# Kernel optimization log

Measured on AMD Instinct MI355X. Metric: run time of the kernel, lower is better.

The kernel has to match this reference:

```python
import math
import jax, jax.numpy as jnp
import numpy as np

CHUNK = 32
EPS = 1e-5


def l2norm(x):
    return x * jax.lax.rsqrt(jnp.sum(x * x, -1, keepdims=True))


def causal_dwconv(x, w):
    # x: (B, C, L); w: (C, K) depthwise causal conv (left pad K-1)
    C, K = w.shape
    return jax.lax.conv_general_dilated(x, w[:, None, :], (1,), [(K - 1, 0)], feature_group_count=C)


def per_head_stats(x):
    # x: (B,L,H,D) -> (B,L,H,4): mean, var(pop), abs-mean, l2-norm
    mean = jnp.mean(x, -1, keepdims=True)
    var = jnp.mean(x * x, -1, keepdims=True) - mean * mean
    abs_mean = jnp.mean(jnp.abs(x), -1, keepdims=True)
    l2 = jnp.sqrt(jnp.sum(x * x, -1, keepdims=True))
    return jnp.concatenate([mean, var, abs_mean, l2], -1)


def delta_rule_chunkwise(q, k, v, beta, chunk=CHUNK):
    # q,k: (B,H,L,dk); v: (B,H,L,dv); beta: (B,H,L)
    b, h, L, dk = q.shape
    dv = v.shape[-1]
    pad = (-L) % chunk
    if pad:
        pc = ((0, 0), (0, 0), (0, pad), (0, 0))
        q, k, v = (jnp.pad(t, pc) for t in (q, k, v))
        beta = jnp.pad(beta, ((0, 0), (0, 0), (0, pad)))
    Lp = L + pad
    n = Lp // chunk
    q = l2norm(q)
    k = l2norm(k)
    v = v * beta[..., None]
    kb = k * beta[..., None]
    resh = lambda t: t.reshape(b, h, n, chunk, t.shape[-1])
    q, k, v, kb = map(resh, (q, k, v, kb))
    tri = jnp.triu(jnp.ones((chunk, chunk), bool))          # incl. diag
    strict = jnp.triu(jnp.ones((chunk, chunk), bool), 1)    # above diag
    A = jnp.where(tri, 0.0, -jnp.einsum('bhncd,bhned->bhnce', kb, k))
    # forward-substitution inverse of (I - strict_lower) as in the torch loop
    for i in range(1, chunk):
        upd = jnp.einsum('...k,...kj->...j', A[..., i, :], A[..., :, :i])
        A = A.at[..., i, :i].add(upd)
    inv = A + jnp.eye(chunk, dtype=A.dtype)
    u = inv @ v   # (b,h,n,c,dv)
    w = inv @ kb  # (b,h,n,c,dk)

    def step(S, xs):
        qi, ki, ui, wi = xs  # (b,h,c,d)
        attn = jnp.where(strict, 0.0, qi @ jnp.swapaxes(ki, -1, -2))
        u_adj = ui - wi @ S
        out_i = qi @ S + attn @ u_adj
        S = S + jnp.swapaxes(ki, -1, -2) @ u_adj
        return S, out_i

    xs = tuple(jnp.moveaxis(t, 2, 0) for t in (q, k, u, w))
    S0 = jnp.zeros((b, h, dk, dv), q.dtype)
    S, outs = jax.lax.scan(step, S0, xs)
    out = jnp.moveaxis(outs, 0, 2).reshape(b, h, Lp, dv)[:, :, :L]
    return out, S


def reference(hidden_states, q_proj_w, k_proj_w, v_proj_w, b_proj_w,
              q_conv_w, k_conv_w, v_conv_w, fir_short_w, fir_long_w,
              fuse_w1, fuse_b1, fuse_w2, fuse_b2, logit_temp,
              res_scale_short, res_scale_long, o_norm_w, o_proj_w):
    B, L, D = hidden_states.shape
    H = fir_short_w.shape[0]

    def shortconv(x, w):  # x: (B,L,C)
        y = causal_dwconv(jnp.swapaxes(x, 1, 2), w)
        return jax.nn.silu(jnp.swapaxes(y, 1, 2))

    q = shortconv(hidden_states @ q_proj_w.T, q_conv_w)
    k = shortconv(hidden_states @ k_proj_w.T, k_conv_w)
    v = shortconv(hidden_states @ v_proj_w.T, v_conv_w)
    q = q.reshape(B, L, H, -1)
    k = k.reshape(B, L, H, -1)
    v_direct = v.reshape(B, L, H, -1)
    beta = jax.nn.sigmoid(hidden_states @ b_proj_w.T)  # (B,L,H)

    delta_out, _S = delta_rule_chunkwise(
        jnp.transpose(q, (0, 2, 1, 3)), jnp.transpose(k, (0, 2, 1, 3)),
        jnp.transpose(v_direct, (0, 2, 1, 3)), jnp.transpose(beta, (0, 2, 1)))
    delta_out = jnp.transpose(delta_out, (0, 2, 1, 3))

    def fir(x, filt):  # x: (B,L,H,Dh); filt: (H,Dh,K)
        hh, dd, kk = filt.shape
        xf = jnp.swapaxes(x.reshape(B, L, hh * dd), 1, 2)
        y = causal_dwconv(xf, filt.reshape(hh * dd, kk))
        return jnp.swapaxes(y, 1, 2).reshape(B, L, hh, dd)

    local_short = fir(v_direct, fir_short_w)
    local_long = fir(v_direct, fir_long_w)

    stats = jnp.concatenate([per_head_stats(t) for t in
                             (local_short, local_long, delta_out, v_direct)], -1)  # (B,L,H,16)
    hs_exp = jnp.broadcast_to(hidden_states[:, :, None, :], (B, L, H, D))
    gate_in = jnp.concatenate([hs_exp, stats], -1)
    hdn = jax.nn.gelu(gate_in @ fuse_w1.T + fuse_b1, approximate=False)
    logits = hdn @ fuse_w2.T + fuse_b2  # (B,L,H,4)
    temp = jax.nn.softplus(logit_temp) + 1e-4
    fw = jax.nn.softmax(logits / temp, -1)

    o = (fw[..., 0:1] * local_short + fw[..., 1:2] * local_long
         + fw[..., 2:3] * delta_out + fw[..., 3:4] * v_direct)
    o = o + res_scale_short * local_short + res_scale_long * local_long
    o = o * jax.lax.rsqrt(jnp.mean(o * o, -1, keepdims=True) + EPS) * o_norm_w
    return o.reshape(B, L, -1) @ o_proj_w.T


def setup_inputs() -> dict:
    key = jax.random.key(0)
    ks = jax.random.split(key, 16)
    B, L, D, H = 2, 4096, 1024, 4
    dk, dv = D, D
    dh = dv // H
    gate_in_dim = D + 16
    gate_hidden = D * 2 // 2
    s = 0.02
    f32 = jnp.float32
    return {
        'hidden_states': jax.random.normal(ks[0], (B, L, D), f32),
        'q_proj_w': jax.random.normal(ks[1], (dk, D), f32) * s,
        'k_proj_w': jax.random.normal(ks[2], (dk, D), f32) * s,
        'v_proj_w': jax.random.normal(ks[3], (dv, D), f32) * s,
        'b_proj_w': jax.random.normal(ks[4], (H, D), f32) * s,
        'q_conv_w': jax.random.normal(ks[5], (dk, 4), f32) * 0.1,
        'k_conv_w': jax.random.normal(ks[6], (dk, 4), f32) * 0.1,
        'v_conv_w': jax.random.normal(ks[7], (dv, 4), f32) * 0.1,
        'fir_short_w': jax.random.normal(ks[8], (H, dh, 5), f32) * 0.02,
        'fir_long_w': jax.random.normal(ks[9], (H, dh, 64), f32) * 0.02,
        'fuse_w1': jax.random.normal(ks[10], (gate_hidden, gate_in_dim), f32) * s,
        'fuse_b1': jnp.zeros((gate_hidden,), f32),
        'fuse_w2': jax.random.normal(ks[11], (4, gate_hidden), f32) * s,
        'fuse_b2': jnp.array([-1.0, -1.0, 1.0, 3.0], f32),
        'logit_temp': jnp.full((1,), math.log(math.expm1(0.7)), f32),
        'res_scale_short': jnp.full((1,), 0.1, f32),
        'res_scale_long': jnp.full((1,), 0.1, f32),
        'o_norm_w': jnp.ones((dh,), f32),
        'o_proj_w': jax.random.normal(ks[12], (D, dv), f32) * s,
    }
```

## Files before the change

### kernel.cpp

```cpp
#include <hip/hip_runtime.h>
#include <hip/hip_bf16.h>

#define BB 2
#define LL 4096
#define DD 1024
#define HH 4
#define DH 256
#define CH 32
#define NC (LL/CH)
#define BL (BB*LL)
#define BLD ((size_t)BB*LL*DD)

typedef __attribute__((ext_vector_type(8))) short short8;
typedef __attribute__((ext_vector_type(4))) float floatx4;

__device__ __forceinline__ float bf2f(unsigned short u) {
    union { float f; unsigned int i; } x; x.i = ((unsigned int)u) << 16; return x.f;
}
__device__ __forceinline__ float bflo(unsigned int u) {
    union { float f; unsigned int i; } x; x.i = u << 16; return x.f;
}
__device__ __forceinline__ float bfhi(unsigned int u) {
    union { float f; unsigned int i; } x; x.i = u & 0xFFFF0000u; return x.f;
}
__device__ __forceinline__ unsigned short f2bf(float f) {
    union { float f; unsigned int i; } x; x.f = f;
    unsigned int r = x.i + 0x7FFFu + ((x.i >> 16) & 1u);
    return (unsigned short)(r >> 16);
}
__device__ __forceinline__ unsigned int pkbf(float a, float b) {
    unsigned int ua = __float_as_uint(a) + 0x8000u;
    unsigned int ub = __float_as_uint(b) + 0x8000u;
    return __builtin_amdgcn_perm(ub, ua, 0x07060302);
}
__device__ __forceinline__ void lds_barrier() {
    __builtin_amdgcn_s_waitcnt(0xC07F);
    __builtin_amdgcn_s_barrier();
}

typedef __attribute__((address_space(1))) const unsigned int as1_uint;
typedef __attribute__((address_space(3))) unsigned int as3_uint;
__device__ __forceinline__ void dma16(const void* g, void* l) {
    __builtin_amdgcn_global_load_lds((as1_uint*)g, (as3_uint*)l, 16, 0, 0);
}

__global__ __launch_bounds__(256) void cvt_bf_k(
    const float* __restrict__ x, unsigned short* __restrict__ y)
{
    size_t i = ((size_t)blockIdx.x * 256 + threadIdx.x) * 4;
    float4 v = *(const float4*)(x + i);
    ushort4 o;
    o.x = f2bf(v.x); o.y = f2bf(v.y); o.z = f2bf(v.z); o.w = f2bf(v.w);
    *(ushort4*)(y + i) = o;
}

__global__ __launch_bounds__(256) void w1s_prep_k(
    const float* __restrict__ w1, unsigned short* __restrict__ w1s)
{
    int idx = blockIdx.x * 256 + threadIdx.x;
    int e = idx >> 4, s = idx & 15;
    w1s[idx] = f2bf(w1[(size_t)e * 1040 + 1024 + s]);
}

__global__ __launch_bounds__(256) void gemm_mfma(
    const float* __restrict__ A, int lda,
    const float* __restrict__ W, int ldw,
    const float* __restrict__ bias,
    float* __restrict__ C, int ldc, int K)
{
    __shared__ unsigned short Abuf[128][56];
    __shared__ unsigned short Bbuf[128][56];
    const int t = threadIdx.x;
    const int wave = t >> 6, lane = t & 63;
    const int wm = wave >> 1, wn = wave & 1;
    const int row0 = blockIdx.y * 128, col0 = blockIdx.x * 128;

    floatx4 acc[4][4];
#pragma unroll
    for (int i = 0; i < 4; ++i)
#pragma unroll
        for (int j = 0; j < 4; ++j) acc[i][j] = (floatx4){0.f, 0.f, 0.f, 0.f};

    const int fr = lane & 15, fk = (lane >> 4) * 8;

    for (int kt = 0; kt < K; kt += 32) {
        __syncthreads();
#pragma unroll
        for (int it = 0; it < 2; ++it) {
            int idx = t + it * 256;
            int r = idx >> 2, s = (idx & 3) * 8;
            const float* ap = A + (size_t)(row0 + r) * lda + kt + s;
            float4 a0 = *(const float4*)(ap);
            float4 a1 = *(const float4*)(ap + 4);
            ushort4 p0, p1;
            p0.x = f2bf(a0.x); p0.y = f2bf(a0.y); p0.z = f2bf(a0.z); p0.w = f2bf(a0.w);
            p1.x = f2bf(a1.x); p1.y = f2bf(a1.y); p1.z = f2bf(a1.z); p1.w = f2bf(a1.w);
            *(ushort4*)&Abuf[r][s]     = p0;
            *(ushort4*)&Abuf[r][s + 4] = p1;
            const float* wp = W + (size_t)(col0 + r) * ldw + kt + s;
            float4 b0 = *(const float4*)(wp);
            float4 b1 = *(const float4*)(wp + 4);
            ushort4 q0, q1;
            q0.x = f2bf(b0.x); q0.y = f2bf(b0.y); q0.z = f2bf(b0.z); q0.w = f2bf(b0.w);
            q1.x = f2bf(b1.x); q1.y = f2bf(b1.y); q1.z = f2bf(b1.z); q1.w = f2bf(b1.w);
            *(ushort4*)&Bbuf[r][s]     = q0;
            *(ushort4*)&Bbuf[r][s + 4] = q1;
        }
        __syncthreads();

        short8 afrag[4], bfrag[4];
#pragma unroll
        for (int i = 0; i < 4; ++i) {
            afrag[i] = *(const short8*)&Abuf[wm * 64 + i * 16 + fr][fk];
            bfrag[i] = *(const short8*)&Bbuf[wn * 64 + i * 16 + fr][fk];
        }
#pragma unroll
        for (int i = 0; i < 4; ++i)
#pragma unroll
            for (int j = 0; j < 4; ++j)
                acc[i][j] = __builtin_amdgcn_mfma_f32_16x16x32_bf16(
                    afrag[i], bfrag[j], acc[i][j], 0, 0, 0);
    }

    const int fc = lane & 15, frow = (lane >> 4) * 4;
#pragma unroll
    for (int j = 0; j < 4; ++j) {
        int col = col0 + wn * 64 + j * 16 + fc;
        float bv = bias ? bias[col] : 0.0f;
#pragma unroll
        for (int i = 0; i < 4; ++i) {
#pragma unroll
            for (int r = 0; r < 4; ++r) {
                int row = row0 + wm * 64 + i * 16 + frow + r;
                C[(size_t)row * ldc + col] = acc[i][j][r] + bv;
            }
        }
    }
}

__global__ __launch_bounds__(256) void gemm_bb(
    const unsigned short* __restrict__ A, int lda,
    const unsigned short* __restrict__ B, int ldb,
    float* __restrict__ C, int ldc, int K)
{
    __shared__ unsigned short Abuf[128][56];
    __shared__ unsigned short Bbuf[128][56];
    const int t = threadIdx.x;
    const int wave = t >> 6, lane = t & 63;
    const int wm = wave >> 1, wn = wave & 1;
    const int row0 = blockIdx.y * 128, col0 = blockIdx.x * 128;

    floatx4 acc[4][4];
#pragma unroll
    for (int i = 0; i < 4; ++i)
#pragma unroll
        for (int j = 0; j < 4; ++j) acc[i][j] = (floatx4){0.f, 0.f, 0.f, 0.f};

    const int fr = lane & 15, fk = (lane >> 4) * 8;

    for (int kt = 0; kt < K; kt += 32) {
        __syncthreads();
#pragma unroll
        for (int it = 0; it < 2; ++it) {
            int idx = t + it * 256;
            int r = idx >> 2, s = (idx & 3) * 8;
            uint4 av = *(const uint4*)(A + (size_t)(row0 + r) * lda + kt + s);
            *(uint4*)&Abuf[r][s] = av;
            uint4 bv = *(const uint4*)(B + (size_t)(col0 + r) * ldb + kt + s);
            *(uint4*)&Bbuf[r][s] = bv;
        }
        __syncthreads();

        short8 afrag[4], bfrag[4];
#pragma unroll
        for (int i = 0; i < 4; ++i) {
            afrag[i] = *(const short8*)&Abuf[wm * 64 + i * 16 + fr][fk];
            bfrag[i] = *(const short8*)&Bbuf[wn * 64 + i * 16 + fr][fk];
        }
#pragma unroll
        for (int i = 0; i < 4; ++i)
#pragma unroll
            for (int j = 0; j < 4; ++j)
                acc[i][j] = __builtin_amdgcn_mfma_f32_16x16x32_bf16(
                    afrag[i], bfrag[j], acc[i][j], 0, 0, 0);
    }

    const int fc = lane & 15, frow = (lane >> 4) * 4;
#pragma unroll
    for (int j = 0; j < 4; ++j) {
        int col = col0 + wn * 64 + j * 16 + fc;
#pragma unroll
        for (int i = 0; i < 4; ++i) {
#pragma unroll
            for (int r = 0; r < 4; ++r) {
                int row = row0 + wm * 64 + i * 16 + frow + r;
                C[(size_t)row * ldc + col] = acc[i][j][r];
            }
        }
    }
}

__global__ __launch_bounds__(256) void convnorm_qk_k(
    const float* __restrict__ x, const float* __restrict__ w,
    unsigned short* __restrict__ y)
{
    int bl = blockIdx.x >> 2;
    int h  = blockIdx.x & 3;
    int l  = bl & (LL - 1);
    int d  = threadIdx.x;
    int c  = h * DH + d;
    const float* wp = w + (size_t)c * 4;
    const float* xp = x + (size_t)bl * DD + c;
    float acc = wp[3] * xp[0];
    if (l >= 1) acc += wp[2] * xp[-(int)DD];
    if (l >= 2) acc += wp[1] * xp[-2*(int)DD];
    if (l >= 3) acc += wp[0] * xp[-3*(int)DD];
    acc = acc / (1.0f + expf(-acc));
    float s = acc * acc;
#pragma unroll
    for (int off = 32; off > 0; off >>= 1) s += __shfl_down(s, off);
    __shared__ float red[4];
    int wv = threadIdx.x >> 6, ln = threadIdx.x & 63;
    if (ln == 0) red[wv] = s;
    __syncthreads();
    float tot = red[0] + red[1] + red[2] + red[3];
    y[(size_t)bl * DD + c] = f2bf(acc * rsqrtf(tot));
}

__global__ __launch_bounds__(256) void conv_silu_k(
    const float* __restrict__ x, const float* __restrict__ w, float* __restrict__ y)
{
    size_t idx = (size_t)blockIdx.x * 256 + threadIdx.x;
    int c = (int)(idx & (DD - 1));
    int bl = (int)(idx >> 10);
    int l = bl & (LL - 1);
    const float* wp = w + (size_t)c * 4;
    const float* xp = x + (size_t)bl * DD + c;
    float acc = wp[3] * xp[0];
    if (l >= 1) acc += wp[2] * xp[-(int)DD];
    if (l >= 2) acc += wp[1] * xp[-2*(int)DD];
    if (l >= 3) acc += wp[0] * xp[-3*(int)DD];
    y[idx] = acc / (1.0f + expf(-acc));
}

template<int K>
__global__ __launch_bounds__(256) void fir2_k(
    const float* __restrict__ x, const float* __restrict__ filt, float* __restrict__ y)
{
    const int ctile = blockIdx.x & 15;
    const int ltile = (blockIdx.x >> 4) & 63;
    const int b = blockIdx.x >> 10;
    const int RT = 64 + K - 1;
    __shared__ float xs[RT][64];
    __shared__ float fs[64][K + 1];
    const int t = threadIdx.x;
    const int l0 = ltile * 64;

    for (int i = t; i < RT * 16; i += 256) {
        int li = i >> 4, c4 = (i & 15) * 4;
        int l = l0 - (K - 1) + li;
        float4 v = make_float4(0.f, 0.f, 0.f, 0.f);
        if (l >= 0)
            v = *(const float4*)(x + ((size_t)b * LL + l) * DD + ctile * 64 + c4);
        *(float4*)&xs[li][c4] = v;
    }
    for (int i = t; i < 64 * K; i += 256) {
        fs[i / K][i % K] = filt[(size_t)ctile * 64 * K + i];
    }
    __syncthreads();

    const int c = t & 63, lg = t >> 6;
    float acc[16];
#pragma unroll
    for (int o = 0; o < 16; ++o) acc[o] = 0.f;
#pragma unroll
    for (int j = 0; j < 16 + K - 1; ++j) {
        float xv = xs[lg * 16 + j][c];
#pragma unroll
        for (int o = 0; o < 16; ++o) {
            int tap = j - o;
            if (tap >= 0 && tap < K) acc[o] += fs[c][tap] * xv;
        }
    }
    size_t base = ((size_t)b * LL + l0 + lg * 16) * DD + ctile * 64 + c;
#pragma unroll
    for (int o = 0; o < 16; ++o)
        y[base + (size_t)o * DD] = acc[o];
}

__global__ __launch_bounds__(256) void beta_k(
    const float* __restrict__ hs, const float* __restrict__ bw, float* __restrict__ beta)
{
    int bl = blockIdx.x;
    const float* xr = hs + (size_t)bl * DD;
    float a0=0.f,a1=0.f,a2=0.f,a3=0.f;
    for (int k = threadIdx.x; k < DD; k += 256) {
        float xv = xr[k];
        a0 += xv * bw[k];
        a1 += xv * bw[DD + k];
        a2 += xv * bw[2*DD + k];
        a3 += xv * bw[3*DD + k];
    }
#pragma unroll
    for (int off = 32; off > 0; off >>= 1) {
        a0 += __shfl_down(a0, off); a1 += __shfl_down(a1, off);
        a2 += __shfl_down(a2, off); a3 += __shfl_down(a3, off);
    }
    __shared__ float red[4][4];
    int wv = threadIdx.x >> 6, ln = threadIdx.x & 63;
    if (ln == 0) { red[wv][0]=a0; red[wv][1]=a1; red[wv][2]=a2; red[wv][3]=a3; }
    __syncthreads();
    if (threadIdx.x < 4) {
        int h = threadIdx.x;
        float s = red[0][h] + red[1][h] + red[2][h] + red[3][h];
        beta[(size_t)bl * HH + h] = 1.0f / (1.0f + expf(-s));
    }
}

__global__ __launch_bounds__(256) void tr_k(
    const unsigned short* __restrict__ k, unsigned short* __restrict__ kT)
{
    int et = blockIdx.x & 3;
    int lt = (blockIdx.x >> 2) & 63;
    int bh = blockIdx.x >> 8;
    int h = bh & 3, b = bh >> 2;
    __shared__ unsigned short tile[64][72];
    int t = threadIdx.x;
    int tr = t >> 4;
    int tc = (t & 15) * 4;
#pragma unroll
    for (int i = 0; i < 4; ++i) {
        int l = tr + i * 16;
        ushort4 v = *(const ushort4*)(k + ((size_t)b * LL + lt*64 + l) * DD + h * DH + et*64 + tc);
        *(ushort4*)&tile[l][tc] = v;
    }
    __syncthreads();
#pragma unroll
    for (int i = 0; i < 4; ++i) {
        int e = tr + i * 16;
        ushort4 v;
        v.x = tile[tc+0][e]; v.y = tile[tc+1][e];
        v.z = tile[tc+2][e]; v.w = tile[tc+3][e];
        *(ushort4*)(kT + ((size_t)bh * DH + et*64 + e) * LL + (size_t)lt*64 + tc) = v;
    }
}

__global__ __launch_bounds__(256) void chunk_prep2_k(
    const unsigned short* __restrict__ q, const unsigned short* __restrict__ k,
    const unsigned short* __restrict__ kT, const float* __restrict__ v,
    const float* __restrict__ beta,
    unsigned short* __restrict__ uT, unsigned short* __restrict__ w_out,
    unsigned short* __restrict__ attn_out)
{
    const int ci = blockIdx.x & (NC - 1);
    const int bh = blockIdx.x >> 7;
    const int h = bh & (HH - 1), b = bh >> 2;
    __shared__ unsigned short kL[32][264];
    __shared__ unsigned short qL[32][264];
    __shared__ float vL[32][260];
    __shared__ float AmL[32][33];
    __shared__ unsigned short AbH[32][40];
    __shared__ unsigned short AbL2[32][40];
    __shared__ float betL[32];
    const int t = threadIdx.x;
    const int wave = t >> 6, lane = t & 63;
    const int lr = lane & 15, lg = lane >> 4;
    const int l0 = ci * CH;
    const size_t rowbase = (size_t)b * LL + l0;

    for (int i = t; i < 1024; i += 256) {
        int r = i >> 5, s8 = (i & 31) * 8;
        *(uint4*)&kL[r][s8] = *(const uint4*)(k + (rowbase + r) * DD + h * DH + s8);
        *(uint4*)&qL[r][s8] = *(const uint4*)(q + (rowbase + r) * DD + h * DH + s8);
    }
    for (int i = t; i < 2048; i += 256) {
        int e = i >> 6, d4 = (i & 63) * 4;
        *(float4*)&vL[e][d4] = *(const float4*)(v + (rowbase + e) * DD + h * DH + d4);
    }
    if (t < 32) betL[t] = beta[(rowbase + t) * HH + h];
    __syncthreads();

    const int mt = wave >> 1, nt = wave & 1;
    floatx4 accA = (floatx4){0.f,0.f,0.f,0.f}, accT = accA;
#pragma unroll
    for (int ks = 0; ks < 8; ++ks) {
        short8 bk = *(const short8*)&kL[nt * 16 + lr][ks * 32 + lg * 8];
        short8 ak = *(const short8*)&kL[mt * 16 + lr][ks * 32 + lg * 8];
        short8 aq = *(const short8*)&qL[mt * 16 + lr][ks * 32 + lg * 8];
        accA = __builtin_amdgcn_mfma_f32_16x16x32_bf16(ak, bk, accA, 0, 0, 0);
        accT = __builtin_amdgcn_mfma_f32_16x16x32_bf16(aq, bk, accT, 0, 0, 0);
    }
    {
        const size_t abase = (size_t)blockIdx.x * (CH * CH);
        const int ee = nt * 16 + lr;
#pragma unroll
        for (int r = 0; r < 4; ++r) {
            int c = mt * 16 + lg * 4 + r;
            float bc = betL[c];
            AmL[c][ee] = (ee < c) ? (-bc * accA[r]) : 0.0f;
            attn_out[abase + (size_t)c * CH + ee] =
                (ee <= c) ? f2bf(accT[r]) : (unsigned short)0;
        }
    }
    __syncthreads();

    const unsigned short* kTg = kT + (size_t)bh * DH * LL;
    short8 wB[4];
#pragma unroll
    for (int n = 0; n < 4; ++n)
        wB[n] = *(const short8*)(kTg + (size_t)(wave * 64 + n * 16 + lr) * LL + l0 + lg * 8);

    if (wave == 0) {
        const int j = lane & 31;
        float col[32];
#pragma unroll
        for (int c = 0; c < 32; ++c) col[c] = AmL[c][j];
#pragma unroll
        for (int i = 1; i < 32; ++i) {
            float u0 = 0.f, u1 = 0.f;
#pragma unroll
            for (int kk = 0; kk < 32; kk += 2) {
                if (kk < i)     u0 += __shfl(col[i], kk) * col[kk];
                if (kk + 1 < i) u1 += __shfl(col[i], kk + 1) * col[kk + 1];
            }
            if (j < i) col[i] += u0 + u1;
        }
        if (lane < 32) {
            const float bj = betL[j];
#pragma unroll
            for (int c = 0; c < 32; ++c) {
                float val = (col[c] + (c == j ? 1.0f : 0.0f)) * bj;
                unsigned short hi = f2bf(val);
                AbH[c][j] = hi;
                AbL2[c][j] = f2bf(val - bf2f(hi));
            }
        }
    }
    __syncthreads();

    short8 AH[2], ALo[2];
#pragma unroll
    for (int m = 0; m < 2; ++m) {
        AH[m]  = *(const short8*)&AbH[m * 16 + lr][lg * 8];
        ALo[m] = *(const short8*)&AbL2[m * 16 + lr][lg * 8];
    }
    const size_t uTbase = (size_t)bh * DH * LL;
    const size_t wbase  = (size_t)bh * LL * DH;
#pragma unroll
    for (int n = 0; n < 4; ++n) {
        const int d = wave * 64 + n * 16 + lr;
        union { short8 s8; unsigned int u[4]; } vf;
#pragma unroll
        for (int p2 = 0; p2 < 4; ++p2)
            vf.u[p2] = pkbf(vL[lg * 8 + p2 * 2][d], vL[lg * 8 + p2 * 2 + 1][d]);
#pragma unroll
        for (int m = 0; m < 2; ++m) {
            floatx4 au = (floatx4){0.f,0.f,0.f,0.f};
            au = __builtin_amdgcn_mfma_f32_16x16x32_bf16(AH[m],  vf.s8, au, 0, 0, 0);
            au = __builtin_amdgcn_mfma_f32_16x16x32_bf16(ALo[m], vf.s8, au, 0, 0, 0);
            ushort4 ou;
            ou.x = f2bf(au[0]); ou.y = f2bf(au[1]); ou.z = f2bf(au[2]); ou.w = f2bf(au[3]);
            *(ushort4*)(uT + uTbase + (size_t)d * LL + l0 + m * 16 + lg * 4) = ou;

            floatx4 aw = (floatx4){0.f,0.f,0.f,0.f};
            aw = __builtin_amdgcn_mfma_f32_16x16x32_bf16(AH[m],  wB[n], aw, 0, 0, 0);
            aw = __builtin_amdgcn_mfma_f32_16x16x32_bf16(ALo[m], wB[n], aw, 0, 0, 0);
#pragma unroll
            for (int r = 0; r < 4; ++r)
                w_out[wbase + (size_t)(l0 + m * 16 + lg * 4 + r) * DH + d] = f2bf(aw[r]);
        }
    }
}

__global__ __launch_bounds__(256, 1) void scan10_k(
    const unsigned short* __restrict__ q, const unsigned short* __restrict__ kT,
    const unsigned short* __restrict__ uT, const unsigned short* __restrict__ w,
    const unsigned short* __restrict__ attn, float* __restrict__ dout)
{
    const int bh = blockIdx.x & 7;
    const int jb = blockIdx.x >> 3;
    const int h = bh & (HH - 1), b = bh >> 2;
    const int jcol = jb * 16;
    const int wave = threadIdx.x >> 6, lane = threadIdx.x & 63;
    const int lr = lane & 15, lg = lane >> 4;
    const int half = wave & 1;
    const bool isQ = wave >= 2;

    #define OW 0
    #define OQ 16384
    #define OK2 32768
    #define OA 49152
    #define OU 51200
    __shared__ char slotmem[2][52224];
    __shared__ unsigned short SbT[2][16][264];
    __shared__ unsigned short uadjT[2][16][40];

    floatx4 Sacc[4];
#pragma unroll
    for (int mt = 0; mt < 4; ++mt) Sacc[mt] = (floatx4){0.f,0.f,0.f,0.f};

    const char* wbB  = (const char*)(w  + (size_t)bh * LL * DH);
    const char* qbB  = (const char*)(q  + (size_t)b * LL * DD + h * DH);
    const char* kbB  = (const char*)(kT + (size_t)bh * DH * LL);
    const char* uTbB = (const char*)(uT + (size_t)bh * DH * LL);
    const char* atB  = (const char*)(attn + (size_t)bh * NC * (CH * CH));
    float* db = dout + (size_t)bh * LL * DH;

    const int lane16 = lane * 16;
    int pw[4], pq[4], pkt[4];
#pragma unroll
    for (int j = 0; j < 4; ++j) {
        int i = wave + 4 * j;
        int L = i * 1024 + lane16;
        { int row = L >> 9, g = (L >> 4) & 31, gs = g ^ (row & 7);
          pw[j] = row * 512 + gs * 16; }
        { int row = L >> 9, g = (L >> 4) & 31, gs = g ^ (row & 7);
          pq[j] = row * 2048 + gs * 16; }
        { int row = L >> 6, g = (L >> 4) & 3, gs = g ^ (row & 3);
          pkt[j] = row * 8192 + gs * 16; }
    }
    int pat = 0, put = 0;
    if (wave < 2) { int L = wave * 1024 + lane16;
        int row = L >> 6, g = (L >> 4) & 3, gs = g ^ (row & 3);
        pat = row * 64 + gs * 16; }
    else if (wave == 2) { int L = lane16;
        int row = L >> 6, g = (L >> 4) & 3;
        put = (jcol + row) * 8192 + g * 16; }

    const int row_o = half * 16 + lr;
    int opo[8];
#pragma unroll
    for (int kt = 0; kt < 8; ++kt)
        opo[kt] = row_o * 512 + (((kt * 4 + lg) ^ (row_o & 7)) * 16);
    int opk[4];
#pragma unroll
    for (int mt = 0; mt < 4; ++mt) {
        int rk = 64 * wave + 16 * mt + lr;
        opk[mt] = rk * 64 + ((lg ^ (rk & 3)) * 16);
    }
    const int opa = row_o * 64 + ((lg ^ (row_o & 3)) * 16);
    const int opu = lr * 64 + half * 32 + lg * 8;

    {
        char* sb = &slotmem[0][0];
#pragma unroll
        for (int j = 0; j < 4; ++j) {
            int i = wave + 4 * j;
            dma16(wbB + pw[j],  sb + OW  + i * 1024);
            dma16(qbB + pq[j],  sb + OQ  + i * 1024);
            dma16(kbB + pkt[j], sb + OK2 + i * 1024);
        }
        if (wave < 2)       dma16(atB + pat,  sb + OA + wave * 1024);
        else if (wave == 2) dma16(uTbB + put, sb + OU);
    }

#pragma unroll 2
    for (int ci = 0; ci < NC; ++ci) {
        const int p = ci & 1;
        const int l0 = ci * CH;

#pragma unroll
        for (int mt = 0; mt < 4; ++mt) {
            int e0 = 64 * wave + 16 * mt + lg * 4;
            *(unsigned int*)&SbT[p][lr][e0]     = pkbf(Sacc[mt][0], Sacc[mt][1]);
            *(unsigned int*)&SbT[p][lr][e0 + 2] = pkbf(Sacc[mt][2], Sacc[mt][3]);
        }

        asm volatile("s_waitcnt vmcnt(0)" ::: "memory");
        lds_barrier();

        {
            const int cn = (ci + 1 < NC) ? (ci + 1) : ci;
            const size_t lnW = (size_t)(cn * CH) * 512;
            const size_t lnQ = (size_t)(cn * CH) * 2048;
            const size_t lnK = (size_t)(cn * CH) * 2;
            char* sb = &slotmem[p ^ 1][0];
#pragma unroll
            for (int j = 0; j < 4; ++j) {
                int i = wave + 4 * j;
                dma16(wbB + lnW + pw[j],  sb + OW  + i * 1024);
                dma16(qbB + lnQ + pq[j],  sb + OQ  + i * 1024);
                dma16(kbB + lnK + pkt[j], sb + OK2 + i * 1024);
            }
            if (wave < 2)       dma16(atB + (size_t)cn * 2048 + pat, sb + OA + wave * 1024);
            else if (wave == 2) dma16(uTbB + lnK + put, sb + OU);
        }

        const char* sp = &slotmem[p][0];
        const char* ab = sp + (isQ ? OQ : OW);

        floatx4 Pa = (floatx4){0.f,0.f,0.f,0.f}, Pb = Pa;
#pragma unroll
        for (int kt = 0; kt < 4; ++kt) {
            short8 s0 = *(const short8*)&SbT[p][lr][(2*kt)   * 32 + lg * 8];
            short8 s1 = *(const short8*)&SbT[p][lr][(2*kt+1) * 32 + lg * 8];
            short8 a0 = *(const short8*)(ab + opo[2*kt]);
            short8 a1 = *(const short8*)(ab + opo[2*kt+1]);
            Pa = __builtin_amdgcn_mfma_f32_16x16x32_bf16(a0, s0, Pa, 0,0,0);
            Pb = __builtin_amdgcn_mfma_f32_16x16x32_bf16(a1, s1, Pb, 0,0,0);
        }
        floatx4 P = Pa + Pb;

        if (!isQ) {
            ushort4 u4 = *(const ushort4*)(sp + OU + opu);
            float ua0 = bf2f(u4.x) - P[0];
            float ua1 = bf2f(u4.y) - P[1];
            float ua2 = bf2f(u4.z) - P[2];
            float ua3 = bf2f(u4.w) - P[3];
            int cc0 = half * 16 + lg * 4;
            *(unsigned int*)&uadjT[p][lr][cc0]     = pkbf(ua0, ua1);
            *(unsigned int*)&uadjT[p][lr][cc0 + 2] = pkbf(ua2, ua3);
        }
        lds_barrier();

        short8 ub = *(const short8*)&uadjT[p][lr][lg * 8];

        if (isQ) {
            short8 paR = *(const short8*)(sp + OA + opa);
            floatx4 Ot = __builtin_amdgcn_mfma_f32_16x16x32_bf16(paR, ub, P, 0,0,0);
#pragma unroll
            for (int r = 0; r < 4; ++r)
                db[(size_t)(l0 + half * 16 + lg * 4 + r) * DH + jcol + lr] = Ot[r];
        }

#pragma unroll
        for (int mt = 0; mt < 4; ++mt) {
            short8 pkR = *(const short8*)(sp + OK2 + opk[mt]);
            Sacc[mt] = __builtin_amdgcn_mfma_f32_16x16x32_bf16(pkR, ub, Sacc[mt], 0,0,0);
        }
    }
    #undef OW
    #undef OQ
    #undef OK2
    #undef OA
    #undef OU
}

__global__ __launch_bounds__(256) void stats_k(
    const float* __restrict__ ls, const float* __restrict__ llb,
    const float* __restrict__ dox, const float* __restrict__ v,
    float* __restrict__ stats)
{
    int bl = blockIdx.x;
    int b = bl >> 12, l = bl & (LL - 1);
    int wv = threadIdx.x >> 6, ln = threadIdx.x & 63;
    size_t ibase = (size_t)bl * DD + wv * DH;
    size_t dbase = (((size_t)(b * HH + wv)) * LL + l) * DH;
#pragma unroll
    for (int tn = 0; tn < 4; ++tn) {
        const float* p; size_t base;
        if (tn == 0)      { p = ls;  base = ibase; }
        else if (tn == 1) { p = llb; base = ibase; }
        else if (tn == 2) { p = dox; base = dbase; }
        else              { p = v;   base = ibase; }
        float4 x = *(const float4*)(p + base + ln * 4);
        float sm = x.x + x.y + x.z + x.w;
        float sq = x.x*x.x + x.y*x.y + x.z*x.z + x.w*x.w;
        float sa = fabsf(x.x) + fabsf(x.y) + fabsf(x.z) + fabsf(x.w);
#pragma unroll
        for (int off = 32; off > 0; off >>= 1) {
            sm += __shfl_down(sm, off);
            sq += __shfl_down(sq, off);
            sa += __shfl_down(sa, off);
        }
        if (ln == 0) {
            float mean = sm * (1.0f / DH);
            float var = sq * (1.0f / DH) - mean * mean;
            float am = sa * (1.0f / DH);
            float l2 = sqrtf(sq);
            *(float4*)(stats + (size_t)bl * 64 + wv * 16 + tn * 4) =
                make_float4(mean, var, am, l2);
        }
    }
}

__global__ __launch_bounds__(256) void gate_fin2_k(
    const float* __restrict__ hpart, const float* __restrict__ stats,
    const unsigned short* __restrict__ w1s,
    const float* __restrict__ w2, const float* __restrict__ b2,
    const float* __restrict__ ltemp, float* __restrict__ fw)
{
    const int bl = blockIdx.x;
    const int t = threadIdx.x;
    const float temp = log1pf(expf(ltemp[0])) + 1e-4f;
    __shared__ float st[HH][16];
    __shared__ float red[4][16];
    __shared__ float fin[16];
    if (t < 64) st[t >> 4][t & 15] = stats[(size_t)bl * 64 + t];

    const int e0 = t * 4;
    float4 hp4 = *(const float4*)(hpart + (size_t)bl * DD + e0);
    float hp[4] = {hp4.x, hp4.y, hp4.z, hp4.w};
    float w2a[4][4];
#pragma unroll
    for (int j = 0; j < 4; ++j) {
        float4 wv = *(const float4*)(w2 + (size_t)j * 1024 + e0);
        w2a[j][0] = wv.x; w2a[j][1] = wv.y; w2a[j][2] = wv.z; w2a[j][3] = wv.w;
    }
    uint4 wpk[8];
    const uint4* wp = (const uint4*)(w1s + (size_t)e0 * 16);
#pragma unroll
    for (int i = 0; i < 8; ++i) wpk[i] = wp[i];
    __syncthreads();

    float lg[4][4];
#pragma unroll
    for (int h = 0; h < 4; ++h)
#pragma unroll
        for (int j = 0; j < 4; ++j) lg[h][j] = 0.0f;

#pragma unroll
    for (int ii = 0; ii < 4; ++ii) {
        float xh[4] = {hp[ii], hp[ii], hp[ii], hp[ii]};
        unsigned arr[8] = {wpk[ii*2].x, wpk[ii*2].y, wpk[ii*2].z, wpk[ii*2].w,
                           wpk[ii*2+1].x, wpk[ii*2+1].y, wpk[ii*2+1].z, wpk[ii*2+1].w};
#pragma unroll
        for (int p = 0; p < 8; ++p) {
            float wlo = bflo(arr[p]), whi = bfhi(arr[p]);
            int s = p * 2;
#pragma unroll
            for (int h = 0; h < 4; ++h)
                xh[h] += st[h][s] * wlo + st[h][s + 1] * whi;
        }
#pragma unroll
        for (int h = 0; h < 4; ++h) {
            float x = xh[h];
            float gct = 0.5f * x * (1.0f + erff(x * 0.70710678118654752f));
            lg[h][0] += gct * w2a[0][ii];
            lg[h][1] += gct * w2a[1][ii];
            lg[h][2] += gct * w2a[2][ii];
            lg[h][3] += gct * w2a[3][ii];
        }
    }

#pragma unroll
    for (int h = 0; h < 4; ++h)
#pragma unroll
        for (int j = 0; j < 4; ++j)
#pragma unroll
            for (int off = 32; off > 0; off >>= 1)
                lg[h][j] += __shfl_down(lg[h][j], off);

    const int wv = t >> 6, ln = t & 63;
    if (ln == 0) {
#pragma unroll
        for (int h = 0; h < 4; ++h)
#pragma unroll
            for (int j = 0; j < 4; ++j) red[wv][h * 4 + j] = lg[h][j];
    }
    __syncthreads();
    if (t < 16) {
        float s = red[0][t] + red[1][t] + red[2][t] + red[3][t] + b2[t & 3];
        fin[t] = s / temp;
    }
    __syncthreads();
    if (t < 4) {
        float l0 = fin[t*4], l1 = fin[t*4+1], l2 = fin[t*4+2], l3 = fin[t*4+3];
        float m = fmaxf(fmaxf(l0, l1), fmaxf(l2, l3));
        float e0x = expf(l0-m), e1 = expf(l1-m), e2 = expf(l2-m), e3 = expf(l3-m);
        float inv = 1.0f / (e0x + e1 + e2 + e3);
        *(float4*)(fw + (size_t)bl * 16 + t * 4) = make_float4(e0x*inv, e1*inv, e2*inv, e3*inv);
    }
}

__global__ __launch_bounds__(256) void combine_k(
    const float* __restrict__ ls, const float* __restrict__ llb,
    const float* __restrict__ dox, const float* __restrict__ v,
    const float* __restrict__ fw, const float* __restrict__ rss,
    const float* __restrict__ rsl, const float* __restrict__ onw,
    float* __restrict__ opre)
{
    int h = blockIdx.x & (HH - 1);
    int bl = blockIdx.x >> 2;
    int b = bl >> 12, l = bl & (LL - 1);
    int d = threadIdx.x;
    size_t i1 = (size_t)blockIdx.x * DH + d;
    size_t i2 = (((size_t)(b * HH + h)) * LL + l) * DH + d;
    const float* fwp = fw + (size_t)blockIdx.x * 4;
    float f0 = fwp[0], f1 = fwp[1], f2 = fwp[2], f3 = fwp[3];
    float aS = rss[0], aL = rsl[0];
    float vls = ls[i1], vll = llb[i1], vd = dox[i2], vv = v[i1];
    float o = f0*vls + f1*vll + f2*vd + f3*vv + aS*vls + aL*vll;
    float s = o * o;
#pragma unroll
    for (int off = 32; off > 0; off >>= 1) s += __shfl_down(s, off);
    __shared__ float red[4];
    int wv = threadIdx.x >> 6, ln = threadIdx.x & 63;
    if (ln == 0) red[wv] = s;
    __syncthreads();
    float ms = (red[0] + red[1] + red[2] + red[3]) * (1.0f / DH);
    opre[(size_t)bl * DD + h * DH + d] = o * rsqrtf(ms + 1e-5f) * onw[d];
}

extern "C" void kernel_launch(void* const* d_in, const int* in_sizes, int n_in,
                              void* d_out, int out_size, void* d_ws, size_t ws_size,
                              hipStream_t stream)
{
    const float* hs  = (const float*)d_in[0];
    const float* qw  = (const float*)d_in[1];
    const float* kw  = (const float*)d_in[2];
    const float* vw  = (const float*)d_in[3];
    const float* bw  = (const float*)d_in[4];
    const float* qcw = (const float*)d_in[5];
    const float* kcw = (const float*)d_in[6];
    const float* vcw = (const float*)d_in[7];
    const float* fsw = (const float*)d_in[8];
    const float* flw = (const float*)d_in[9];
    const float* w1  = (const float*)d_in[10];
    const float* b1  = (const float*)d_in[11];
    const float* w2  = (const float*)d_in[12];
    const float* b2  = (const float*)d_in[13];
    const float* lt  = (const float*)d_in[14];
    const float* rss = (const float*)d_in[15];
    const float* rsl = (const float*)d_in[16];
    const float* onw = (const float*)d_in[17];
    const float* opw = (const float*)d_in[18];
    float* out = (float*)d_out;

    float* wsf = (float*)d_ws;
    float* tmp   = wsf;
    unsigned short* ktbuf = (unsigned short*)tmp;
    unsigned short* uTbuf = (unsigned short*)(wsf + BLD/2);
    float* vbuf  = wsf + BLD;
    float* dbuf  = wsf + 2*BLD;
    unsigned short* hsb = (unsigned short*)(wsf + 2*BLD);
    unsigned short* qwb = (unsigned short*)(wsf + 2*BLD + BLD/2);
    unsigned short* kwb = qwb + (size_t)DD*DD;
    unsigned short* vwb = kwb + (size_t)DD*DD;
    unsigned short* qbuf = (unsigned short*)(wsf + 3*BLD);
    unsigned short* kbuf = qbuf + BLD;
    float* hpart = wsf + 3*BLD;
    float* opre  = wsf + 3*BLD;
    unsigned short* ubuf = (unsigned short*)(wsf + 4*BLD);
    unsigned short* wbuf = ubuf + BLD;
    float* llbuf = wsf + 4*BLD;
    float* lsbuf = tmp;
    unsigned short* attnb = (unsigned short*)(wsf + 5*BLD);
    float* statsb = wsf + 5*BLD + 524288;
    float* fwbuf  = statsb + (size_t)BL*HH*16;
    float* betab  = fwbuf + (size_t)BL*HH*4;
    unsigned short* w1sp = (unsigned short*)(betab + (size_t)BL*HH);

    dim3 gg(8, 64);

    cvt_bf_k<<<(int)(BLD/1024), 256, 0, stream>>>(hs, hsb);
    cvt_bf_k<<<1024, 256, 0, stream>>>(qw, qwb);
    cvt_bf_k<<<1024, 256, 0, stream>>>(kw, kwb);
    cvt_bf_k<<<1024, 256, 0, stream>>>(vw, vwb);
    w1s_prep_k<<<64, 256, 0, stream>>>(w1, w1sp);

    gemm_bb<<<gg, 256, 0, stream>>>(hsb, DD, qwb, DD, tmp, DD, DD);
    convnorm_qk_k<<<BL*HH, 256, 0, stream>>>(tmp, qcw, qbuf);
    gemm_bb<<<gg, 256, 0, stream>>>(hsb, DD, kwb, DD, tmp, DD, DD);
    convnorm_qk_k<<<BL*HH, 256, 0, stream>>>(tmp, kcw, kbuf);
    gemm_bb<<<gg, 256, 0, stream>>>(hsb, DD, vwb, DD, tmp, DD, DD);
    conv_silu_k<<<(int)(BLD/256), 256, 0, stream>>>(tmp, vcw, vbuf);

    beta_k<<<BL, 256, 0, stream>>>(hs, bw, betab);

    tr_k<<<8*64*4, 256, 0, stream>>>(kbuf, ktbuf);
    chunk_prep2_k<<<BB*HH*NC, 256, 0, stream>>>(qbuf, kbuf, ktbuf, vbuf, betab,
                                                uTbuf, wbuf, attnb);

    scan10_k<<<BB*HH*16, 256, 0, stream>>>(qbuf, ktbuf, uTbuf, wbuf, attnb, dbuf);

    fir2_k<5><<<BB*64*16, 256, 0, stream>>>(vbuf, fsw, lsbuf);
    fir2_k<64><<<BB*64*16, 256, 0, stream>>>(vbuf, flw, llbuf);

    stats_k<<<BL, 256, 0, stream>>>(lsbuf, llbuf, dbuf, vbuf, statsb);

    gemm_mfma<<<gg, 256, 0, stream>>>(hs, DD, w1, 1040, b1, hpart, DD, DD);
    gate_fin2_k<<<BL, 256, 0, stream>>>(hpart, statsb, w1sp, w2, b2, lt, fwbuf);

    combine_k<<<BL*HH, 256, 0, stream>>>(lsbuf, llbuf, dbuf, vbuf, fwbuf, rss, rsl, onw, opre);

    gemm_mfma<<<gg, 256, 0, stream>>>(opre, DD, opw, DD, nullptr, out, DD, DD);
}
```

Baseline: 876.4 us.

## Prefetch scan operands into registers instead of LDS DMA double buffering

The chunk scan kernel no longer stages w/q/kT/attn/uT tiles through LDS with global_load_lds. Each wave now loads exactly the fragments it needs directly into registers, double-buffered one chunk ahead, and uses partial vmcnt waits so the next chunk's loads overlap the current compute. The aim is to cut LDS traffic, drop the full vmcnt(0) drain and shrink shared memory. In exchange, register pressure rises (two sets of 13 short8 fragments per thread), global accesses become less coalesced, and the hand-counted vmcnt values are fragile.

```diff
diff --git a/kernel.cpp b/kernel.cpp
--- a/kernel.cpp
+++ b/kernel.cpp
@@ -37,11 +37,15 @@
     __builtin_amdgcn_s_waitcnt(0xC07F);
     __builtin_amdgcn_s_barrier();
 }
-
-typedef __attribute__((address_space(1))) const unsigned int as1_uint;
-typedef __attribute__((address_space(3))) unsigned int as3_uint;
-__device__ __forceinline__ void dma16(const void* g, void* l) {
-    __builtin_amdgcn_global_load_lds((as1_uint*)g, (as3_uint*)l, 16, 0, 0);
+__device__ __forceinline__ short8 gload16(const void* p) {
+    short8 r;
+    asm volatile("global_load_dwordx4 %0, %1, off" : "=v"(r) : "v"(p) : "memory");
+    return r;
+}
+__device__ __forceinline__ uint2 gload8(const void* p) {
+    uint2 r;
+    asm volatile("global_load_dwordx2 %0, %1, off" : "=v"(r) : "v"(p) : "memory");
+    return r;
 }
 
 __global__ __launch_bounds__(256) void cvt_bf_k(
@@ -472,7 +476,7 @@
     }
 }
 
-__global__ __launch_bounds__(256, 1) void scan10_k(
+__global__ __launch_bounds__(256, 1) void scan12_k(
     const unsigned short* __restrict__ q, const unsigned short* __restrict__ kT,
     const unsigned short* __restrict__ uT, const unsigned short* __restrict__ w,
     const unsigned short* __restrict__ attn, float* __restrict__ dout)
@@ -486,154 +490,104 @@
     const int half = wave & 1;
     const bool isQ = wave >= 2;
 
-    #define OW 0
-    #define OQ 16384
-    #define OK2 32768
-    #define OA 49152
-    #define OU 51200
-    __shared__ char slotmem[2][52224];
-    __shared__ unsigned short SbT[2][16][264];
-    __shared__ unsigned short uadjT[2][16][40];
+    __shared__ unsigned short SbT[16][264];
+    __shared__ unsigned short uadjT[16][40];
 
     floatx4 Sacc[4];
 #pragma unroll
     for (int mt = 0; mt < 4; ++mt) Sacc[mt] = (floatx4){0.f,0.f,0.f,0.f};
 
-    const char* wbB  = (const char*)(w  + (size_t)bh * LL * DH);
-    const char* qbB  = (const char*)(q  + (size_t)b * LL * DD + h * DH);
-    const char* kbB  = (const char*)(kT + (size_t)bh * DH * LL);
-    const char* uTbB = (const char*)(uT + (size_t)bh * DH * LL);
-    const char* atB  = (const char*)(attn + (size_t)bh * NC * (CH * CH));
+    const unsigned short* qb  = q + (size_t)b * LL * DD + h * DH;
+    const unsigned short* wb  = w + (size_t)bh * LL * DH;
+    const unsigned short* ob  = isQ ? qb : wb;
+    const size_t ost          = isQ ? (size_t)DD : (size_t)DH;
+    const unsigned short* orow0 = ob + (size_t)(half * 16 + lr) * ost + lg * 8;
+    const unsigned short* kTb = kT + (size_t)bh * DH * LL
+                                + (size_t)(64 * wave + lr) * LL + lg * 8;
+    const unsigned short* uTb = uT + ((size_t)bh * DH + jcol + lr) * LL + half * 16 + lg * 4;
+    const unsigned short* atb = attn + (size_t)bh * NC * (CH * CH)
+                                + (size_t)(half * 16 + lr) * CH + lg * 8;
     float* db = dout + (size_t)bh * LL * DH;
 
-    const int lane16 = lane * 16;
-    int pw[4], pq[4], pkt[4];
-#pragma unroll
-    for (int j = 0; j < 4; ++j) {
-        int i = wave + 4 * j;
-        int L = i * 1024 + lane16;
-        { int row = L >> 9, g = (L >> 4) & 31, gs = g ^ (row & 7);
-          pw[j] = row * 512 + gs * 16; }
-        { int row = L >> 9, g = (L >> 4) & 31, gs = g ^ (row & 7);
-          pq[j] = row * 2048 + gs * 16; }
-        { int row = L >> 6, g = (L >> 4) & 3, gs = g ^ (row & 3);
-          pkt[j] = row * 8192 + gs * 16; }
-    }
-    int pat = 0, put = 0;
-    if (wave < 2) { int L = wave * 1024 + lane16;
-        int row = L >> 6, g = (L >> 4) & 3, gs = g ^ (row & 3);
-        pat = row * 64 + gs * 16; }
-    else if (wave == 2) { int L = lane16;
-        int row = L >> 6, g = (L >> 4) & 3;
-        put = (jcol + row) * 8192 + g * 16; }
-
-    const int row_o = half * 16 + lr;
-    int opo[8];
-#pragma unroll
-    for (int kt = 0; kt < 8; ++kt)
-        opo[kt] = row_o * 512 + (((kt * 4 + lg) ^ (row_o & 7)) * 16);
-    int opk[4];
-#pragma unroll
-    for (int mt = 0; mt < 4; ++mt) {
-        int rk = 64 * wave + 16 * mt + lr;
-        opk[mt] = rk * 64 + ((lg ^ (rk & 3)) * 16);
-    }
-    const int opa = row_o * 64 + ((lg ^ (row_o & 3)) * 16);
-    const int opu = lr * 64 + half * 32 + lg * 8;
-
-    {
-        char* sb = &slotmem[0][0];
-#pragma unroll
-        for (int j = 0; j < 4; ++j) {
-            int i = wave + 4 * j;
-            dma16(wbB + pw[j],  sb + OW  + i * 1024);
-            dma16(qbB + pq[j],  sb + OQ  + i * 1024);
-            dma16(kbB + pkt[j], sb + OK2 + i * 1024);
-        }
-        if (wave < 2)       dma16(atB + pat,  sb + OA + wave * 1024);
-        else if (wave == 2) dma16(uTbB + put, sb + OU);
-    }
+    short8 po[2][8];
+    short8 pk[2][4];
+    short8 pa[2];
+    uint2  pu[2];
+
+#define ISSUE13(cn, s)                                                          \
+    {                                                                           \
+        const int ln_ = (cn) * CH;                                              \
+        const unsigned short* orow_ = orow0 + (size_t)ln_ * ost;                \
+        po[s][0] = gload16(orow_ + 0*32);  po[s][1] = gload16(orow_ + 1*32);    \
+        po[s][2] = gload16(orow_ + 2*32);  po[s][3] = gload16(orow_ + 3*32);    \
+        po[s][4] = gload16(orow_ + 4*32);  po[s][5] = gload16(orow_ + 5*32);    \
+        po[s][6] = gload16(orow_ + 6*32);  po[s][7] = gload16(orow_ + 7*32);    \
+        pk[s][0] = gload16(kTb + (size_t)(0*16) * LL + ln_);                    \
+        pk[s][1] = gload16(kTb + (size_t)(1*16) * LL + ln_);                    \
+        pk[s][2] = gload16(kTb + (size_t)(2*16) * LL + ln_);                    \
+        pk[s][3] = gload16(kTb + (size_t)(3*16) * LL + ln_);                    \
+        if (!isQ) pu[s] = gload8(uTb + ln_);                                    \
+        else      pa[s] = gload16(atb + (size_t)(cn) * (CH * CH));              \
+    }
+
+    ISSUE13(0, 0);
 
 #pragma unroll 2
     for (int ci = 0; ci < NC; ++ci) {
         const int p = ci & 1;
         const int l0 = ci * CH;
 
+        {
+            const int cn = (ci + 1 < NC) ? (ci + 1) : ci;
+            ISSUE13(cn, p ^ 1);
+        }
+
 #pragma unroll
         for (int mt = 0; mt < 4; ++mt) {
             int e0 = 64 * wave + 16 * mt + lg * 4;
-            *(unsigned int*)&SbT[p][lr][e0]     = pkbf(Sacc[mt][0], Sacc[mt][1]);
-            *(unsigned int*)&SbT[p][lr][e0 + 2] = pkbf(Sacc[mt][2], Sacc[mt][3]);
-        }
-
-        asm volatile("s_waitcnt vmcnt(0)" ::: "memory");
+            *(uint2*)&SbT[lr][e0] = make_uint2(pkbf(Sacc[mt][0], Sacc[mt][1]),
+                                               pkbf(Sacc[mt][2], Sacc[mt][3]));
+        }
         lds_barrier();
 
-        {
-            const int cn = (ci + 1 < NC) ? (ci + 1) : ci;
-            const size_t lnW = (size_t)(cn * CH) * 512;
-            const size_t lnQ = (size_t)(cn * CH) * 2048;
-            const size_t lnK = (size_t)(cn * CH) * 2;
-            char* sb = &slotmem[p ^ 1][0];
-#pragma unroll
-            for (int j = 0; j < 4; ++j) {
-                int i = wave + 4 * j;
-                dma16(wbB + lnW + pw[j],  sb + OW  + i * 1024);
-                dma16(qbB + lnQ + pq[j],  sb + OQ  + i * 1024);
-                dma16(kbB + lnK + pkt[j], sb + OK2 + i * 1024);
-            }
-            if (wave < 2)       dma16(atB + (size_t)cn * 2048 + pat, sb + OA + wave * 1024);
-            else if (wave == 2) dma16(uTbB + lnK + put, sb + OU);
-        }
-
-        const char* sp = &slotmem[p][0];
-        const char* ab = sp + (isQ ? OQ : OW);
+        if (!isQ || ci == 0) { asm volatile("s_waitcnt vmcnt(13)" ::: "memory"); }
+        else                 { asm volatile("s_waitcnt vmcnt(17)" ::: "memory"); }
+        __builtin_amdgcn_sched_barrier(0);
 
         floatx4 Pa = (floatx4){0.f,0.f,0.f,0.f}, Pb = Pa;
 #pragma unroll
         for (int kt = 0; kt < 4; ++kt) {
-            short8 s0 = *(const short8*)&SbT[p][lr][(2*kt)   * 32 + lg * 8];
-            short8 s1 = *(const short8*)&SbT[p][lr][(2*kt+1) * 32 + lg * 8];
-            short8 a0 = *(const short8*)(ab + opo[2*kt]);
-            short8 a1 = *(const short8*)(ab + opo[2*kt+1]);
-            Pa = __builtin_amdgcn_mfma_f32_16x16x32_bf16(a0, s0, Pa, 0,0,0);
-            Pb = __builtin_amdgcn_mfma_f32_16x16x32_bf16(a1, s1, Pb, 0,0,0);
+            short8 s0 = *(const short8*)&SbT[lr][(2*kt)   * 32 + lg * 8];
+            short8 s1 = *(const short8*)&SbT[lr][(2*kt+1) * 32 + lg * 8];
+            Pa = __builtin_amdgcn_mfma_f32_16x16x32_bf16(po[p][2*kt],   s0, Pa, 0,0,0);
+            Pb = __builtin_amdgcn_mfma_f32_16x16x32_bf16(po[p][2*kt+1], s1, Pb, 0,0,0);
         }
         floatx4 P = Pa + Pb;
 
         if (!isQ) {
-            ushort4 u4 = *(const ushort4*)(sp + OU + opu);
-            float ua0 = bf2f(u4.x) - P[0];
-            float ua1 = bf2f(u4.y) - P[1];
-            float ua2 = bf2f(u4.z) - P[2];
-            float ua3 = bf2f(u4.w) - P[3];
+            float ua0 = bflo(pu[p].x) - P[0];
+            float ua1 = bfhi(pu[p].x) - P[1];
+            float ua2 = bflo(pu[p].y) - P[2];
+            float ua3 = bfhi(pu[p].y) - P[3];
             int cc0 = half * 16 + lg * 4;
-            *(unsigned int*)&uadjT[p][lr][cc0]     = pkbf(ua0, ua1);
-            *(unsigned int*)&uadjT[p][lr][cc0 + 2] = pkbf(ua2, ua3);
+            *(uint2*)&uadjT[lr][cc0] = make_uint2(pkbf(ua0, ua1), pkbf(ua2, ua3));
         }
         lds_barrier();
 
-        short8 ub = *(const short8*)&uadjT[p][lr][lg * 8];
+        short8 ub = *(const short8*)&uadjT[lr][lg * 8];
 
         if (isQ) {
-            short8 paR = *(const short8*)(sp + OA + opa);
-            floatx4 Ot = __builtin_amdgcn_mfma_f32_16x16x32_bf16(paR, ub, P, 0,0,0);
+            floatx4 Ot = __builtin_amdgcn_mfma_f32_16x16x32_bf16(pa[p], ub, P, 0,0,0);
 #pragma unroll
             for (int r = 0; r < 4; ++r)
                 db[(size_t)(l0 + half * 16 + lg * 4 + r) * DH + jcol + lr] = Ot[r];
         }
 
 #pragma unroll
-        for (int mt = 0; mt < 4; ++mt) {
-            short8 pkR = *(const short8*)(sp + OK2 + opk[mt]);
-            Sacc[mt] = __builtin_amdgcn_mfma_f32_16x16x32_bf16(pkR, ub, Sacc[mt], 0,0,0);
-        }
-    }
-    #undef OW
-    #undef OQ
-    #undef OK2
-    #undef OA
-    #undef OU
+        for (int mt = 0; mt < 4; ++mt)
+            Sacc[mt] = __builtin_amdgcn_mfma_f32_16x16x32_bf16(pk[p][mt], ub, Sacc[mt], 0,0,0);
+    }
+#undef ISSUE13
 }
 
 __global__ __launch_bounds__(256) void stats_k(
@@ -862,7 +816,7 @@
     chunk_prep2_k<<<BB*HH*NC, 256, 0, stream>>>(qbuf, kbuf, ktbuf, vbuf, betab,
                                                 uTbuf, wbuf, attnb);
 
-    scan10_k<<<BB*HH*16, 256, 0, stream>>>(qbuf, ktbuf, uTbuf, wbuf, attnb, dbuf);
+    scan12_k<<<BB*HH*16, 256, 0, stream>>>(qbuf, ktbuf, uTbuf, wbuf, attnb, dbuf);
 
     fir2_k<5><<<BB*64*16, 256, 0, stream>>>(vbuf, fsw, lsbuf);
     fir2_k<64><<<BB*64*16, 256, 0, stream>>>(vbuf, flw, llbuf);
```

Result: no change. 886.1 us (+1.1%).
